# Optimization experiments

Hardware: AMD Instinct MI355X
Metric: run time of the kernel (lower is better)

The kernel has to match this reference:

```python
import jax, jax.numpy as jnp
import numpy as np

H, Dh = 8, 64          # heads, per-head dim
FEA = H * Dh           # 512
B, T, N = 2, 128, 128
BETA = 0.3
EPS = 1e-5
SEG = T // H


def _ln(x):
    # LayerNorm over last dim, no affine params (elementwise_affine=False)
    m = jnp.mean(x, axis=-1, keepdims=True)
    v = jnp.mean((x - m) ** 2, axis=-1, keepdims=True)
    return (x - m) / jnp.sqrt(v + EPS)


def setup_inputs() -> dict:
    key = jax.random.key(0)
    ks = jax.random.split(key, 10)
    mkw = lambda k: jax.random.normal(k, (FEA, FEA), jnp.float32) * 0.02
    return {
        "x": jax.random.normal(ks[0], (B, T, N, FEA), jnp.float32),
        "te": jax.random.normal(ks[1], (B, T, N, FEA), jnp.float32),
        "Wq": mkw(ks[2]), "bq": jnp.zeros((FEA,), jnp.float32),
        "Wk": mkw(ks[3]), "bk": jnp.zeros((FEA,), jnp.float32),
        "Wv": mkw(ks[4]), "bv": jnp.zeros((FEA,), jnp.float32),
        "Wo": mkw(ks[5]), "bo": jnp.zeros((FEA,), jnp.float32),
        "W1": mkw(ks[6]), "b1": jnp.zeros((FEA,), jnp.float32),
        "W2": mkw(ks[7]), "b2": jnp.zeros((FEA,), jnp.float32),
    }


def reference(x, te, Wq, bq, Wk, bk, Wv, bv, Wo, bo, W1, b1, W2, b2):
    xt = x + te                                        # [B,T,N,F]
    q = (xt @ Wq + bq).reshape(B, T, N, H, Dh)
    k = (xt @ Wk + bk).reshape(B, T, N, H, Dh)
    v = (xt @ Wv + bv).reshape(B, T, N, H, Dh)

    # scores[b,h,n,s,t] = q_s . k_t / sqrt(d)
    scores = jnp.einsum('bsnhd,btnhd->bhnst', q, k) / np.sqrt(Dh).astype(np.float32)

    # causal mask (Mask=True): key t <= query s
    causal = jnp.tril(jnp.ones((T, T), dtype=bool))
    scores = jnp.where(causal[None, None, None], scores, -jnp.inf)

    # segment-focus reweighting (Mask2=True): head i keeps key columns
    # [i*SEG, (i+1)*SEG) (last head extends to T) at full weight, scales
    # everything else by BETA. (-inf * BETA stays -inf.)
    cols = jnp.arange(T)
    start = jnp.arange(H) * SEG
    end = jnp.where(jnp.arange(H) == H - 1, T, start + SEG)
    focus = (cols[None, :] >= start[:, None]) & (cols[None, :] < end[:, None])  # [H,T]
    scores = jnp.where(focus[None, :, None, None, :], scores, scores * BETA)

    attn = jax.nn.softmax(scores, axis=-1)
    out = jnp.einsum('bhnst,btnhd->bsnhd', attn, v).reshape(B, T, N, FEA)

    out = out @ Wo + bo
    out = _ln(out + xt)

    # FeedForward([F,F,F], res_ln=True): linear-relu-linear + residual + LN
    h = jax.nn.relu(out @ W1 + b1)
    h = h @ W2 + b2
    return _ln(h + out)
```

## Files before the change

### kernel.cpp

```cpp
#include <hip/hip_runtime.h>
#include <math.h>

typedef unsigned int uint;
typedef unsigned short ushort;

#define FEA 512
#define NH 8
#define DH 64
#define BB 2
#define TT 128
#define NN 128
#define MTOT (BB*TT*NN)
#define SEG 16
#define BETA 0.3f
#define LNEPS 1e-5f

typedef __attribute__((ext_vector_type(8))) short bf16x8;
typedef __attribute__((ext_vector_type(4))) float f32x4;
typedef __attribute__((ext_vector_type(8))) short s16x8;

static __device__ __forceinline__ ushort f2bf(float x) {
  uint u = __float_as_uint(x);
  return (ushort)((u + 0x7FFFu + ((u >> 16) & 1u)) >> 16);
}
static __device__ __forceinline__ float b2f(short x) {
  return __uint_as_float(((uint)(ushort)x) << 16);
}

__global__ __launch_bounds__(256) void add_fused(const float* __restrict__ x,
                                                 const float* __restrict__ te,
                                                 float* __restrict__ xt,
                                                 ushort* __restrict__ xtb) {
  size_t i = ((size_t)blockIdx.x * 256 + threadIdx.x) * 8;
  float4 a0 = *(const float4*)&x[i];
  float4 a1 = *(const float4*)&x[i + 4];
  float4 b0 = *(const float4*)&te[i];
  float4 b1 = *(const float4*)&te[i + 4];
  float u[8];
  u[0]=a0.x+b0.x; u[1]=a0.y+b0.y; u[2]=a0.z+b0.z; u[3]=a0.w+b0.w;
  u[4]=a1.x+b1.x; u[5]=a1.y+b1.y; u[6]=a1.z+b1.z; u[7]=a1.w+b1.w;
  *(float4*)&xt[i]     = make_float4(u[0],u[1],u[2],u[3]);
  *(float4*)&xt[i + 4] = make_float4(u[4],u[5],u[6],u[7]);
  s16x8 o;
  #pragma unroll
  for (int j = 0; j < 8; ++j) o[j] = (short)f2bf(u[j]);
  *(s16x8*)&xtb[i] = o;
}

struct W6 { const float* s[6]; };

__global__ __launch_bounds__(256) void wconv(W6 w, ushort* __restrict__ dst) {
  __shared__ float t[32][33];
  const float* W = w.s[blockIdx.z];
  ushort* WT = dst + (size_t)blockIdx.z * FEA * FEA;
  const int k0 = blockIdx.y * 32, n0 = blockIdx.x * 32;
  const int tx = threadIdx.x & 31, ty = threadIdx.x >> 5;
  #pragma unroll
  for (int i = 0; i < 4; ++i)
    t[ty + i * 8][tx] = W[(size_t)(k0 + ty + i * 8) * FEA + n0 + tx];
  __syncthreads();
  #pragma unroll
  for (int i = 0; i < 4; ++i)
    WT[(size_t)(n0 + ty + i * 8) * FEA + k0 + tx] = f2bf(t[tx][ty + i * 8]);
}

template<int RELU>
__global__ __launch_bounds__(256) void gemm_bf(const ushort* __restrict__ A,
                                               const ushort* __restrict__ WT,
                                               const float* __restrict__ bias,
                                               ushort* __restrict__ C) {
  __shared__ ushort As[128 * 32];
  __shared__ ushort Bs[128 * 32];
  const int tid = threadIdx.x;
  const int m0 = blockIdx.y * 128;
  const int n0 = blockIdx.x * 128;
  const int lane = tid & 63;
  const int wid = tid >> 6;
  const int wm = wid >> 1, wn = wid & 1;
  const int lrow = lane & 15, lk = lane >> 4;

  f32x4 acc[4][4] = {};

  int r_[2], kq_[2];
  #pragma unroll
  for (int c = 0; c < 2; ++c) {
    int i = c * 256 + tid;
    r_[c] = i >> 2;
    kq_[c] = (i & 3) ^ ((r_[c] >> 1) & 3);
  }

  for (int k0 = 0; k0 < 512; k0 += 32) {
    #pragma unroll
    for (int c = 0; c < 2; ++c) {
      const ushort* ga = A  + (size_t)(m0 + r_[c]) * 512 + k0 + kq_[c] * 8;
      const ushort* gb = WT + (size_t)(n0 + r_[c]) * 512 + k0 + kq_[c] * 8;
      __builtin_amdgcn_global_load_lds(
          (const __attribute__((address_space(1))) void*)ga,
          (__attribute__((address_space(3))) void*)&As[(c * 256 + tid) * 8], 16, 0, 0);
      __builtin_amdgcn_global_load_lds(
          (const __attribute__((address_space(1))) void*)gb,
          (__attribute__((address_space(3))) void*)&Bs[(c * 256 + tid) * 8], 16, 0, 0);
    }
    __syncthreads();

    bf16x8 af[4], bfr[4];
    #pragma unroll
    for (int s = 0; s < 4; ++s) {
      int ra = wm * 64 + s * 16 + lrow;
      int sa = ra * 4 + (lk ^ ((ra >> 1) & 3));
      af[s] = *(const bf16x8*)&As[sa * 8];
      int rb = wn * 64 + s * 16 + lrow;
      int sb = rb * 4 + (lk ^ ((rb >> 1) & 3));
      bfr[s] = *(const bf16x8*)&Bs[sb * 8];
    }
    #pragma unroll
    for (int i = 0; i < 4; ++i)
      #pragma unroll
      for (int j = 0; j < 4; ++j)
        acc[i][j] = __builtin_amdgcn_mfma_f32_16x16x32_bf16(af[i], bfr[j], acc[i][j], 0, 0, 0);
    __syncthreads();
  }

  float bv[4];
  #pragma unroll
  for (int s = 0; s < 4; ++s) bv[s] = bias[n0 + wn * 64 + s * 16 + lrow];
  #pragma unroll
  for (int i = 0; i < 4; ++i) {
    const int grow = m0 + wm * 64 + i * 16 + lk * 4;
    #pragma unroll
    for (int j = 0; j < 4; ++j) {
      const int gcol = n0 + wn * 64 + j * 16 + lrow;
      #pragma unroll
      for (int q = 0; q < 4; ++q) {
        float o = acc[i][j][q] + bv[j];
        if (RELU) o = fmaxf(o, 0.f);
        C[(size_t)(grow + q) * 512 + gcol] = f2bf(o);
      }
    }
  }
}

__global__ __launch_bounds__(256) void attn_mfma(const ushort* __restrict__ kp,
                                                 const ushort* __restrict__ vp,
                                                 ushort* __restrict__ qo) {
  __shared__ ushort Ks[8192];
  __shared__ ushort Vt[8192];
  __shared__ ushort Pb[4][1024];
  __shared__ float  Lb[4][32];

  const int bid = blockIdx.x;
  const int h = bid & 7;
  const int n = (bid >> 3) & 127;
  const int b = bid >> 10;
  const int tid = threadIdx.x;
  const int lane = tid & 63;
  const int w = tid >> 6;
  const int g = lane >> 4, c = lane & 15;
  const size_t tstride = (size_t)NN * FEA;
  const size_t base = ((size_t)b * TT * NN + n) * FEA + (size_t)h * DH;

  #pragma unroll
  for (int it = 0; it < 4; ++it) {
    int i = it * 256 + tid;
    int t = i >> 3;
    int gd = (i & 7) ^ (t & 7);
    const ushort* gk = kp + base + (size_t)t * tstride + gd * 8;
    __builtin_amdgcn_global_load_lds(
        (const __attribute__((address_space(1))) void*)gk,
        (__attribute__((address_space(3))) void*)&Ks[i * 8], 16, 0, 0);
  }
  #pragma unroll
  for (int it = 0; it < 4; ++it) {
    int j = it * 256 + tid;
    int t = j >> 3, d0 = (j & 7) * 8;
    s16x8 vv = *(const s16x8*)&vp[base + (size_t)t * tstride + d0];
    #pragma unroll
    for (int jj = 0; jj < 8; ++jj) {
      int d = d0 + jj;
      int slot = d * 16 + ((t >> 3) ^ (d & 7) ^ (d >> 3));
      Vt[slot * 8 + (t & 7)] = (ushort)vv[jj];
    }
  }
  const int qb = w * 32;
  bf16x8 Qf[2][2];
  #pragma unroll
  for (int qt = 0; qt < 2; ++qt)
    #pragma unroll
    for (int kf = 0; kf < 2; ++kf)
      Qf[qt][kf] = *(const bf16x8*)
          &qo[base + (size_t)(qb + qt * 16 + c) * tstride + kf * 32 + g * 8];
  __syncthreads();

  const int fs = h * SEG;
  const int fe = (h == NH - 1) ? TT : fs + SEG;

  f32x4 Oa[2][4];
  #pragma unroll
  for (int qt = 0; qt < 2; ++qt)
    #pragma unroll
    for (int dt = 0; dt < 4; ++dt)
      Oa[qt][dt] = (f32x4){0.f, 0.f, 0.f, 0.f};
  float lsum[2] = {0.f, 0.f};

  for (int ch = 0; ch <= w; ++ch) {
    const int tc = ch * 32;
    f32x4 sf[2][2];
    #pragma unroll
    for (int tt2 = 0; tt2 < 2; ++tt2) {
      bf16x8 Kf[2];
      #pragma unroll
      for (int kf = 0; kf < 2; ++kf) {
        int t = tc + tt2 * 16 + c;
        int slot = t * 8 + ((kf * 4 + g) ^ (c & 7));
        Kf[kf] = *(const bf16x8*)&Ks[slot * 8];
      }
      #pragma unroll
      for (int qt = 0; qt < 2; ++qt) {
        f32x4 s = (f32x4){0.f, 0.f, 0.f, 0.f};
        s = __builtin_amdgcn_mfma_f32_16x16x32_bf16(Kf[0], Qf[qt][0], s, 0, 0, 0);
        s = __builtin_amdgcn_mfma_f32_16x16x32_bf16(Kf[1], Qf[qt][1], s, 0, 0, 0);
        sf[tt2][qt] = s;
      }
    }
    #pragma unroll
    for (int tt2 = 0; tt2 < 2; ++tt2) {
      #pragma unroll
      for (int qt = 0; qt < 2; ++qt) {
        const int q = qb + qt * 16 + c;
        const int qr = qt * 16 + c;
        #pragma unroll
        for (int pr = 0; pr < 2; ++pr) {
          float pv[2];
          #pragma unroll
          for (int rr = 0; rr < 2; ++rr) {
            int reg = pr * 2 + rr;
            int t = tc + tt2 * 16 + g * 4 + reg;
            float mult = (t >= fs && t < fe) ? 0.125f : 0.125f * BETA;
            float p = __expf(sf[tt2][qt][reg] * mult);
            p = (t <= q) ? p : 0.f;
            pv[rr] = p;
            lsum[qt] += p;
          }
          uint pk = (uint)f2bf(pv[0]) | ((uint)f2bf(pv[1]) << 16);
          int tl = tt2 * 16 + g * 4 + pr * 2;
          int slot = qr * 4 + ((tl >> 3) ^ (qr & 3));
          *(uint*)&Pb[w][slot * 8 + (tl & 7)] = pk;
        }
      }
    }
    bf16x8 Vf[4];
    #pragma unroll
    for (int dt = 0; dt < 4; ++dt) {
      int d = dt * 16 + c;
      int slot = d * 16 + ((((tc >> 3)) + g) ^ (d & 7) ^ (d >> 3));
      Vf[dt] = *(const bf16x8*)&Vt[slot * 8];
    }
    #pragma unroll
    for (int qt = 0; qt < 2; ++qt) {
      int qr = qt * 16 + c;
      int slot = qr * 4 + (g ^ (qr & 3));
      bf16x8 Pa = *(const bf16x8*)&Pb[w][slot * 8];
      #pragma unroll
      for (int dt = 0; dt < 4; ++dt)
        Oa[qt][dt] = __builtin_amdgcn_mfma_f32_16x16x32_bf16(Pa, Vf[dt], Oa[qt][dt], 0, 0, 0);
    }
  }

  #pragma unroll
  for (int qt = 0; qt < 2; ++qt) {
    lsum[qt] += __shfl_xor(lsum[qt], 16, 64);
    lsum[qt] += __shfl_xor(lsum[qt], 32, 64);
  }
  if (g == 0) {
    Lb[w][c]      = 1.0f / lsum[0];
    Lb[w][16 + c] = 1.0f / lsum[1];
  }
  #pragma unroll
  for (int qt = 0; qt < 2; ++qt) {
    f32x4 linv = *(const f32x4*)&Lb[w][qt * 16 + g * 4];
    #pragma unroll
    for (int dt = 0; dt < 4; ++dt) {
      #pragma unroll
      for (int reg = 0; reg < 4; ++reg) {
        int q = qb + qt * 16 + g * 4 + reg;
        qo[base + (size_t)q * tstride + dt * 16 + c] = f2bf(Oa[qt][dt][reg] * linv[reg]);
      }
    }
  }
}

template<int ABF, int RBF, int OBF>
__global__ __launch_bounds__(256) void ln_add(const void* __restrict__ a_,
                                              const void* __restrict__ r_,
                                              void* __restrict__ y_) {
  const int lane = threadIdx.x & 63;
  const int w = threadIdx.x >> 6;
  const size_t row = (size_t)blockIdx.x * 4 + w;
  const size_t off = row * FEA + (size_t)lane * 8;
  float ua[8], ur[8], u[8];
  if (ABF) {
    s16x8 v = *(const s16x8*)&((const ushort*)a_)[off];
    #pragma unroll
    for (int j = 0; j < 8; ++j) ua[j] = b2f(v[j]);
  } else {
    float4 v0 = *(const float4*)&((const float*)a_)[off];
    float4 v1 = *(const float4*)&((const float*)a_)[off + 4];
    ua[0]=v0.x; ua[1]=v0.y; ua[2]=v0.z; ua[3]=v0.w;
    ua[4]=v1.x; ua[5]=v1.y; ua[6]=v1.z; ua[7]=v1.w;
  }
  if (RBF) {
    s16x8 v = *(const s16x8*)&((const ushort*)r_)[off];
    #pragma unroll
    for (int j = 0; j < 8; ++j) ur[j] = b2f(v[j]);
  } else {
    float4 v0 = *(const float4*)&((const float*)r_)[off];
    float4 v1 = *(const float4*)&((const float*)r_)[off + 4];
    ur[0]=v0.x; ur[1]=v0.y; ur[2]=v0.z; ur[3]=v0.w;
    ur[4]=v1.x; ur[5]=v1.y; ur[6]=v1.z; ur[7]=v1.w;
  }
  float sum = 0.f, sq = 0.f;
  #pragma unroll
  for (int j = 0; j < 8; ++j) {
    u[j] = ua[j] + ur[j];
    sum += u[j];
    sq = fmaf(u[j], u[j], sq);
  }
  #pragma unroll
  for (int m = 1; m < 64; m <<= 1) {
    sum += __shfl_xor(sum, m, 64);
    sq  += __shfl_xor(sq,  m, 64);
  }
  const float mean = sum * (1.0f / FEA);
  const float var = sq * (1.0f / FEA) - mean * mean;
  const float rstd = rsqrtf(var + LNEPS);
  if (OBF) {
    s16x8 o;
    #pragma unroll
    for (int j = 0; j < 8; ++j) o[j] = (short)f2bf((u[j] - mean) * rstd);
    *(s16x8*)&((ushort*)y_)[off] = o;
  } else {
    float4 o0, o1;
    o0.x=(u[0]-mean)*rstd; o0.y=(u[1]-mean)*rstd; o0.z=(u[2]-mean)*rstd; o0.w=(u[3]-mean)*rstd;
    o1.x=(u[4]-mean)*rstd; o1.y=(u[5]-mean)*rstd; o1.z=(u[6]-mean)*rstd; o1.w=(u[7]-mean)*rstd;
    *(float4*)&((float*)y_)[off] = o0;
    *(float4*)&((float*)y_)[off + 4] = o1;
  }
}

extern "C" void kernel_launch(void* const* d_in, const int* in_sizes, int n_in,
                              void* d_out, int out_size, void* d_ws, size_t ws_size,
                              hipStream_t stream) {
  const float* x  = (const float*)d_in[0];
  const float* te = (const float*)d_in[1];
  const float* bq = (const float*)d_in[3];
  const float* bk = (const float*)d_in[5];
  const float* bv = (const float*)d_in[7];
  const float* bo = (const float*)d_in[9];
  const float* b1 = (const float*)d_in[11];
  const float* b2 = (const float*)d_in[13];
  float* out = (float*)d_out;

  const size_t E = (size_t)MTOT * FEA;
  ushort* B0 = (ushort*)d_ws;
  ushort* B1 = B0 + E;
  ushort* B2 = B1 + E;
  ushort* B3 = B2 + E;
  ushort* WB = B3 + E;
  const size_t WE = (size_t)FEA * FEA;
  float* xt = out;

  dim3 gGemm(4, 256);

  add_fused<<<E / 8 / 256, 256, 0, stream>>>(x, te, xt, B0);
  W6 w;
  w.s[0] = (const float*)d_in[2];  w.s[1] = (const float*)d_in[4];
  w.s[2] = (const float*)d_in[6];  w.s[3] = (const float*)d_in[8];
  w.s[4] = (const float*)d_in[10]; w.s[5] = (const float*)d_in[12];
  wconv<<<dim3(16, 16, 6), 256, 0, stream>>>(w, WB);
  gemm_bf<0><<<gGemm, 256, 0, stream>>>(B0, WB + 0 * WE, bq, B1);
  gemm_bf<0><<<gGemm, 256, 0, stream>>>(B0, WB + 1 * WE, bk, B2);
  gemm_bf<0><<<gGemm, 256, 0, stream>>>(B0, WB + 2 * WE, bv, B3);
  attn_mfma<<<BB * NN * NH, 256, 0, stream>>>(B2, B3, B1);
  gemm_bf<0><<<gGemm, 256, 0, stream>>>(B1, WB + 3 * WE, bo, B2);
  ln_add<1, 0, 1><<<MTOT / 4, 256, 0, stream>>>(B2, xt, B0);
  gemm_bf<1><<<gGemm, 256, 0, stream>>>(B0, WB + 4 * WE, b1, B3);
  gemm_bf<0><<<gGemm, 256, 0, stream>>>(B3, WB + 5 * WE, b2, B1);
  ln_add<1, 1, 0><<<MTOT / 4, 256, 0, stream>>>(B1, B0, out);
}
```

Baseline: 461.0 us.

## Switch intermediates to fp16, drop fp32 residual copy, vectorize GEMM epilogue stores

Converts all bf16 intermediates and MFMA ops to fp16 and stops writing the fp32 xt copy, reading the residual from the fp16 buffer instead. This removes one full fp32 write and read of the activation tensor. The GEMM operands are swapped so each lane holds four contiguous output columns, allowing packed 8-byte stores and float4 bias loads. The fp16 range and precision of the residual path and of ln_add operating in place on B0 could affect accuracy.

```diff
diff --git a/kernel.cpp b/kernel.cpp
--- a/kernel.cpp
+++ b/kernel.cpp
@@ -15,36 +15,32 @@
 #define BETA 0.3f
 #define LNEPS 1e-5f
 
-typedef __attribute__((ext_vector_type(8))) short bf16x8;
+typedef __attribute__((ext_vector_type(8))) _Float16 f16x8;
 typedef __attribute__((ext_vector_type(4))) float f32x4;
 typedef __attribute__((ext_vector_type(8))) short s16x8;
 
-static __device__ __forceinline__ ushort f2bf(float x) {
-  uint u = __float_as_uint(x);
-  return (ushort)((u + 0x7FFFu + ((u >> 16) & 1u)) >> 16);
-}
-static __device__ __forceinline__ float b2f(short x) {
-  return __uint_as_float(((uint)(ushort)x) << 16);
-}
-
-__global__ __launch_bounds__(256) void add_fused(const float* __restrict__ x,
-                                                 const float* __restrict__ te,
-                                                 float* __restrict__ xt,
-                                                 ushort* __restrict__ xtb) {
+static __device__ __forceinline__ ushort f2h(float x) {
+  _Float16 h = (_Float16)x;
+  return __builtin_bit_cast(ushort, h);
+}
+static __device__ __forceinline__ float h2f(ushort u) {
+  return (float)__builtin_bit_cast(_Float16, u);
+}
+
+__global__ __launch_bounds__(256) void add_h(const float* __restrict__ x,
+                                             const float* __restrict__ te,
+                                             ushort* __restrict__ xth) {
   size_t i = ((size_t)blockIdx.x * 256 + threadIdx.x) * 8;
   float4 a0 = *(const float4*)&x[i];
   float4 a1 = *(const float4*)&x[i + 4];
   float4 b0 = *(const float4*)&te[i];
   float4 b1 = *(const float4*)&te[i + 4];
-  float u[8];
-  u[0]=a0.x+b0.x; u[1]=a0.y+b0.y; u[2]=a0.z+b0.z; u[3]=a0.w+b0.w;
-  u[4]=a1.x+b1.x; u[5]=a1.y+b1.y; u[6]=a1.z+b1.z; u[7]=a1.w+b1.w;
-  *(float4*)&xt[i]     = make_float4(u[0],u[1],u[2],u[3]);
-  *(float4*)&xt[i + 4] = make_float4(u[4],u[5],u[6],u[7]);
   s16x8 o;
-  #pragma unroll
-  for (int j = 0; j < 8; ++j) o[j] = (short)f2bf(u[j]);
-  *(s16x8*)&xtb[i] = o;
+  o[0]=(short)f2h(a0.x+b0.x); o[1]=(short)f2h(a0.y+b0.y);
+  o[2]=(short)f2h(a0.z+b0.z); o[3]=(short)f2h(a0.w+b0.w);
+  o[4]=(short)f2h(a1.x+b1.x); o[5]=(short)f2h(a1.y+b1.y);
+  o[6]=(short)f2h(a1.z+b1.z); o[7]=(short)f2h(a1.w+b1.w);
+  *(s16x8*)&xth[i] = o;
 }
 
 struct W6 { const float* s[6]; };
@@ -61,14 +57,14 @@
   __syncthreads();
   #pragma unroll
   for (int i = 0; i < 4; ++i)
-    WT[(size_t)(n0 + ty + i * 8) * FEA + k0 + tx] = f2bf(t[tx][ty + i * 8]);
+    WT[(size_t)(n0 + ty + i * 8) * FEA + k0 + tx] = f2h(t[tx][ty + i * 8]);
 }
 
 template<int RELU>
-__global__ __launch_bounds__(256) void gemm_bf(const ushort* __restrict__ A,
-                                               const ushort* __restrict__ WT,
-                                               const float* __restrict__ bias,
-                                               ushort* __restrict__ C) {
+__global__ __launch_bounds__(256) void gemm_h(const ushort* __restrict__ A,
+                                              const ushort* __restrict__ WT,
+                                              const float* __restrict__ bias,
+                                              ushort* __restrict__ C) {
   __shared__ ushort As[128 * 32];
   __shared__ ushort Bs[128 * 32];
   const int tid = threadIdx.x;
@@ -77,65 +73,72 @@
   const int lane = tid & 63;
   const int wid = tid >> 6;
   const int wm = wid >> 1, wn = wid & 1;
-  const int lrow = lane & 15, lk = lane >> 4;
+  const int c = lane & 15, g = lane >> 4;
 
   f32x4 acc[4][4] = {};
 
   int r_[2], kq_[2];
   #pragma unroll
-  for (int c = 0; c < 2; ++c) {
-    int i = c * 256 + tid;
-    r_[c] = i >> 2;
-    kq_[c] = (i & 3) ^ ((r_[c] >> 1) & 3);
+  for (int cc = 0; cc < 2; ++cc) {
+    int i = cc * 256 + tid;
+    r_[cc] = i >> 2;
+    kq_[cc] = (i & 3) ^ ((r_[cc] >> 1) & 3);
   }
 
   for (int k0 = 0; k0 < 512; k0 += 32) {
     #pragma unroll
-    for (int c = 0; c < 2; ++c) {
-      const ushort* ga = A  + (size_t)(m0 + r_[c]) * 512 + k0 + kq_[c] * 8;
-      const ushort* gb = WT + (size_t)(n0 + r_[c]) * 512 + k0 + kq_[c] * 8;
+    for (int cc = 0; cc < 2; ++cc) {
+      const ushort* ga = A  + (size_t)(m0 + r_[cc]) * 512 + k0 + kq_[cc] * 8;
+      const ushort* gb = WT + (size_t)(n0 + r_[cc]) * 512 + k0 + kq_[cc] * 8;
       __builtin_amdgcn_global_load_lds(
           (const __attribute__((address_space(1))) void*)ga,
-          (__attribute__((address_space(3))) void*)&As[(c * 256 + tid) * 8], 16, 0, 0);
+          (__attribute__((address_space(3))) void*)&As[(cc * 256 + tid) * 8], 16, 0, 0);
       __builtin_amdgcn_global_load_lds(
           (const __attribute__((address_space(1))) void*)gb,
-          (__attribute__((address_space(3))) void*)&Bs[(c * 256 + tid) * 8], 16, 0, 0);
+          (__attribute__((address_space(3))) void*)&Bs[(cc * 256 + tid) * 8], 16, 0, 0);
     }
     __syncthreads();
 
-    bf16x8 af[4], bfr[4];
+    f16x8 af[4], bfr[4];
     #pragma unroll
     for (int s = 0; s < 4; ++s) {
-      int ra = wm * 64 + s * 16 + lrow;
-      int sa = ra * 4 + (lk ^ ((ra >> 1) & 3));
-      af[s] = *(const bf16x8*)&As[sa * 8];
-      int rb = wn * 64 + s * 16 + lrow;
-      int sb = rb * 4 + (lk ^ ((rb >> 1) & 3));
-      bfr[s] = *(const bf16x8*)&Bs[sb * 8];
+      int ra = wm * 64 + s * 16 + c;
+      int sa = ra * 4 + (g ^ ((ra >> 1) & 3));
+      af[s] = *(const f16x8*)&As[sa * 8];
+      int rb = wn * 64 + s * 16 + c;
+      int sb = rb * 4 + (g ^ ((rb >> 1) & 3));
+      bfr[s] = *(const f16x8*)&Bs[sb * 8];
     }
     #pragma unroll
     for (int i = 0; i < 4; ++i)
       #pragma unroll
       for (int j = 0; j < 4; ++j)
-        acc[i][j] = __builtin_amdgcn_mfma_f32_16x16x32_bf16(af[i], bfr[j], acc[i][j], 0, 0, 0);
+        acc[i][j] = __builtin_amdgcn_mfma_f32_16x16x32_f16(bfr[j], af[i], acc[i][j], 0, 0, 0);
     __syncthreads();
   }
 
-  float bv[4];
-  #pragma unroll
-  for (int s = 0; s < 4; ++s) bv[s] = bias[n0 + wn * 64 + s * 16 + lrow];
+  float4 bv4[4];
+  #pragma unroll
+  for (int j = 0; j < 4; ++j)
+    bv4[j] = *(const float4*)&bias[n0 + wn * 64 + j * 16 + g * 4];
   #pragma unroll
   for (int i = 0; i < 4; ++i) {
-    const int grow = m0 + wm * 64 + i * 16 + lk * 4;
+    const size_t rb = (size_t)(m0 + wm * 64 + i * 16 + c) * 512;
     #pragma unroll
     for (int j = 0; j < 4; ++j) {
-      const int gcol = n0 + wn * 64 + j * 16 + lrow;
-      #pragma unroll
-      for (int q = 0; q < 4; ++q) {
-        float o = acc[i][j][q] + bv[j];
-        if (RELU) o = fmaxf(o, 0.f);
-        C[(size_t)(grow + q) * 512 + gcol] = f2bf(o);
-      }
+      const int nb = n0 + wn * 64 + j * 16 + g * 4;
+      float o0 = acc[i][j][0] + bv4[j].x;
+      float o1 = acc[i][j][1] + bv4[j].y;
+      float o2 = acc[i][j][2] + bv4[j].z;
+      float o3 = acc[i][j][3] + bv4[j].w;
+      if (RELU) {
+        o0 = fmaxf(o0, 0.f); o1 = fmaxf(o1, 0.f);
+        o2 = fmaxf(o2, 0.f); o3 = fmaxf(o3, 0.f);
+      }
+      uint2 pk;
+      pk.x = (uint)f2h(o0) | ((uint)f2h(o1) << 16);
+      pk.y = (uint)f2h(o2) | ((uint)f2h(o3) << 16);
+      *(uint2*)&C[rb + nb] = pk;
     }
   }
 }
@@ -182,12 +185,12 @@
     }
   }
   const int qb = w * 32;
-  bf16x8 Qf[2][2];
+  f16x8 Qf[2][2];
   #pragma unroll
   for (int qt = 0; qt < 2; ++qt)
     #pragma unroll
     for (int kf = 0; kf < 2; ++kf)
-      Qf[qt][kf] = *(const bf16x8*)
+      Qf[qt][kf] = *(const f16x8*)
           &qo[base + (size_t)(qb + qt * 16 + c) * tstride + kf * 32 + g * 8];
   __syncthreads();
 
@@ -207,18 +210,18 @@
     f32x4 sf[2][2];
     #pragma unroll
     for (int tt2 = 0; tt2 < 2; ++tt2) {
-      bf16x8 Kf[2];
+      f16x8 Kf[2];
       #pragma unroll
       for (int kf = 0; kf < 2; ++kf) {
         int t = tc + tt2 * 16 + c;
         int slot = t * 8 + ((kf * 4 + g) ^ (c & 7));
-        Kf[kf] = *(const bf16x8*)&Ks[slot * 8];
+        Kf[kf] = *(const f16x8*)&Ks[slot * 8];
       }
       #pragma unroll
       for (int qt = 0; qt < 2; ++qt) {
         f32x4 s = (f32x4){0.f, 0.f, 0.f, 0.f};
-        s = __builtin_amdgcn_mfma_f32_16x16x32_bf16(Kf[0], Qf[qt][0], s, 0, 0, 0);
-        s = __builtin_amdgcn_mfma_f32_16x16x32_bf16(Kf[1], Qf[qt][1], s, 0, 0, 0);
+        s = __builtin_amdgcn_mfma_f32_16x16x32_f16(Kf[0], Qf[qt][0], s, 0, 0, 0);
+        s = __builtin_amdgcn_mfma_f32_16x16x32_f16(Kf[1], Qf[qt][1], s, 0, 0, 0);
         sf[tt2][qt] = s;
       }
     }
@@ -241,28 +244,28 @@
             pv[rr] = p;
             lsum[qt] += p;
           }
-          uint pk = (uint)f2bf(pv[0]) | ((uint)f2bf(pv[1]) << 16);
+          uint pk = (uint)f2h(pv[0]) | ((uint)f2h(pv[1]) << 16);
           int tl = tt2 * 16 + g * 4 + pr * 2;
           int slot = qr * 4 + ((tl >> 3) ^ (qr & 3));
           *(uint*)&Pb[w][slot * 8 + (tl & 7)] = pk;
         }
       }
     }
-    bf16x8 Vf[4];
+    f16x8 Vf[4];
     #pragma unroll
     for (int dt = 0; dt < 4; ++dt) {
       int d = dt * 16 + c;
       int slot = d * 16 + ((((tc >> 3)) + g) ^ (d & 7) ^ (d >> 3));
-      Vf[dt] = *(const bf16x8*)&Vt[slot * 8];
+      Vf[dt] = *(const f16x8*)&Vt[slot * 8];
     }
     #pragma unroll
     for (int qt = 0; qt < 2; ++qt) {
       int qr = qt * 16 + c;
       int slot = qr * 4 + (g ^ (qr & 3));
-      bf16x8 Pa = *(const bf16x8*)&Pb[w][slot * 8];
+      f16x8 Pa = *(const f16x8*)&Pb[w][slot * 8];
       #pragma unroll
       for (int dt = 0; dt < 4; ++dt)
-        Oa[qt][dt] = __builtin_amdgcn_mfma_f32_16x16x32_bf16(Pa, Vf[dt], Oa[qt][dt], 0, 0, 0);
+        Oa[qt][dt] = __builtin_amdgcn_mfma_f32_16x16x32_f16(Pa, Vf[dt], Oa[qt][dt], 0, 0, 0);
     }
   }
 
@@ -283,13 +286,13 @@
       #pragma unroll
       for (int reg = 0; reg < 4; ++reg) {
         int q = qb + qt * 16 + g * 4 + reg;
-        qo[base + (size_t)q * tstride + dt * 16 + c] = f2bf(Oa[qt][dt][reg] * linv[reg]);
-      }
-    }
-  }
-}
-
-template<int ABF, int RBF, int OBF>
+        qo[base + (size_t)q * tstride + dt * 16 + c] = f2h(Oa[qt][dt][reg] * linv[reg]);
+      }
+    }
+  }
+}
+
+template<int AH, int RH, int OH>
 __global__ __launch_bounds__(256) void ln_add(const void* __restrict__ a_,
                                               const void* __restrict__ r_,
                                               void* __restrict__ y_) {
@@ -298,20 +301,20 @@
   const size_t row = (size_t)blockIdx.x * 4 + w;
   const size_t off = row * FEA + (size_t)lane * 8;
   float ua[8], ur[8], u[8];
-  if (ABF) {
+  if (AH) {
     s16x8 v = *(const s16x8*)&((const ushort*)a_)[off];
     #pragma unroll
-    for (int j = 0; j < 8; ++j) ua[j] = b2f(v[j]);
+    for (int j = 0; j < 8; ++j) ua[j] = h2f((ushort)v[j]);
   } else {
     float4 v0 = *(const float4*)&((const float*)a_)[off];
     float4 v1 = *(const float4*)&((const float*)a_)[off + 4];
     ua[0]=v0.x; ua[1]=v0.y; ua[2]=v0.z; ua[3]=v0.w;
     ua[4]=v1.x; ua[5]=v1.y; ua[6]=v1.z; ua[7]=v1.w;
   }
-  if (RBF) {
+  if (RH) {
     s16x8 v = *(const s16x8*)&((const ushort*)r_)[off];
     #pragma unroll
-    for (int j = 0; j < 8; ++j) ur[j] = b2f(v[j]);
+    for (int j = 0; j < 8; ++j) ur[j] = h2f((ushort)v[j]);
   } else {
     float4 v0 = *(const float4*)&((const float*)r_)[off];
     float4 v1 = *(const float4*)&((const float*)r_)[off + 4];
@@ -333,10 +336,10 @@
   const float mean = sum * (1.0f / FEA);
   const float var = sq * (1.0f / FEA) - mean * mean;
   const float rstd = rsqrtf(var + LNEPS);
-  if (OBF) {
+  if (OH) {
     s16x8 o;
     #pragma unroll
-    for (int j = 0; j < 8; ++j) o[j] = (short)f2bf((u[j] - mean) * rstd);
+    for (int j = 0; j < 8; ++j) o[j] = (short)f2h((u[j] - mean) * rstd);
     *(s16x8*)&((ushort*)y_)[off] = o;
   } else {
     float4 o0, o1;
@@ -367,23 +370,22 @@
   ushort* B3 = B2 + E;
   ushort* WB = B3 + E;
   const size_t WE = (size_t)FEA * FEA;
-  float* xt = out;
 
   dim3 gGemm(4, 256);
 
-  add_fused<<<E / 8 / 256, 256, 0, stream>>>(x, te, xt, B0);
+  add_h<<<E / 8 / 256, 256, 0, stream>>>(x, te, B0);
   W6 w;
   w.s[0] = (const float*)d_in[2];  w.s[1] = (const float*)d_in[4];
   w.s[2] = (const float*)d_in[6];  w.s[3] = (const float*)d_in[8];
   w.s[4] = (const float*)d_in[10]; w.s[5] = (const float*)d_in[12];
   wconv<<<dim3(16, 16, 6), 256, 0, stream>>>(w, WB);
-  gemm_bf<0><<<gGemm, 256, 0, stream>>>(B0, WB + 0 * WE, bq, B1);
-  gemm_bf<0><<<gGemm, 256, 0, stream>>>(B0, WB + 1 * WE, bk, B2);
-  gemm_bf<0><<<gGemm, 256, 0, stream>>>(B0, WB + 2 * WE, bv, B3);
+  gemm_h<0><<<gGemm, 256, 0, stream>>>(B0, WB + 0 * WE, bq, B1);
+  gemm_h<0><<<gGemm, 256, 0, stream>>>(B0, WB + 1 * WE, bk, B2);
+  gemm_h<0><<<gGemm, 256, 0, stream>>>(B0, WB + 2 * WE, bv, B3);
   attn_mfma<<<BB * NN * NH, 256, 0, stream>>>(B2, B3, B1);
-  gemm_bf<0><<<gGemm, 256, 0, stream>>>(B1, WB + 3 * WE, bo, B2);
-  ln_add<1, 0, 1><<<MTOT / 4, 256, 0, stream>>>(B2, xt, B0);
-  gemm_bf<1><<<gGemm, 256, 0, stream>>>(B0, WB + 4 * WE, b1, B3);
-  gemm_bf<0><<<gGemm, 256, 0, stream>>>(B3, WB + 5 * WE, b2, B1);
+  gemm_h<0><<<gGemm, 256, 0, stream>>>(B1, WB + 3 * WE, bo, B2);
+  ln_add<1, 1, 1><<<MTOT / 4, 256, 0, stream>>>(B2, B0, B0);
+  gemm_h<1><<<gGemm, 256, 0, stream>>>(B0, WB + 4 * WE, b1, B3);
+  gemm_h<0><<<gGemm, 256, 0, stream>>>(B3, WB + 5 * WE, b2, B1);
   ln_add<1, 1, 0><<<MTOT / 4, 256, 0, stream>>>(B1, B0, out);
 }
```

Measured after the change: 454.2 us. About the same (-1.5%).
